# Performance work log

Measured on AMD Instinct MI355X. Metric: run time of the kernel, lower is better.

The kernel has to match this reference:

```python
import jax, jax.numpy as jnp
import numpy as np

K = 3  # from init kwarg


def setup_inputs() -> dict:
    key = jax.random.key(0)
    k1, k2 = jax.random.split(key)
    B, N, D = 32, 2048, 128
    features = jax.random.normal(k1, (B, N, D), dtype=jnp.float32)
    strength = jax.random.uniform(k2, (), dtype=jnp.float32)
    return {"features": features, "strength": strength}


def reference(features, strength):
    B, N, D = features.shape
    k = min(K, N - 1)
    x = jax.lax.stop_gradient(features)  # torch uses features.detach() for the mix path

    # pairwise euclidean distance (torch.cdist, p=2): ||a||^2 + ||b||^2 - 2 a.b
    sq = jnp.sum(x * x, axis=-1)                     # (B, N)
    d2 = sq[:, :, None] + sq[:, None, :] - 2.0 * jnp.einsum('bnd,bmd->bnm', x, x)
    dist = jnp.sqrt(jnp.maximum(d2, 0.0))            # (B, N, N)

    # mask self-distance with +1e6 on the diagonal
    eye = jnp.eye(N, dtype=dist.dtype)
    dist = dist + eye[None, :, :] * 1000000.0

    # k smallest -> top_k of negated distances
    _, idx = jax.lax.top_k(-dist, k)                 # idx: (B, N, k)

    # gather neighbor features: gathered[b,n,j] = x[b, idx[b,n,j]]
    gathered = x[jnp.arange(B)[:, None, None], idx]  # (B, N, k, D)
    mix = jnp.mean(gathered, axis=2)                 # (B, N, D)

    s = jnp.clip(strength, 0.0, 1.0)
    return (1.0 - s) * features + s * mix
```

## Files before the change

kernel.cpp:

```cpp
#include <hip/hip_runtime.h>
#include <cfloat>

#define BB 32
#define NN 2048
#define DD 128
#define RM 64
#define CN 64

typedef __attribute__((ext_vector_type(8))) short short8;
typedef __attribute__((ext_vector_type(4))) float float4v;

__device__ __forceinline__ unsigned short f2bf(float f) {
    unsigned int u = __builtin_bit_cast(unsigned int, f);
    u += 0x7FFFu + ((u >> 16) & 1u);
    return (unsigned short)(u >> 16);
}

__device__ __forceinline__ unsigned int umn(unsigned int a, unsigned int b) { return a < b ? a : b; }
__device__ __forceinline__ unsigned int umx(unsigned int a, unsigned int b) { return a > b ? a : b; }
#define CSU(a, b) { unsigned int _lo = umn(a, b), _hi = umx(a, b); (a) = _lo; (b) = _hi; }

__device__ __forceinline__ void gl2lds16(const unsigned short* g, unsigned short* l) {
    __builtin_amdgcn_global_load_lds(
        (const __attribute__((address_space(1))) void*)g,
        (__attribute__((address_space(3))) void*)l, 16, 0, 0);
}

__global__ __launch_bounds__(256) void prep_kernel(const float* __restrict__ x,
        unsigned short* __restrict__ xb16, float* __restrict__ sq) {
    int t = blockIdx.x * 256 + threadIdx.x;
    int row = t >> 2;
    int q = t & 3;
    const float4* xp = reinterpret_cast<const float4*>(x + (size_t)row * DD + q * 32);
    unsigned short* op = xb16 + (size_t)row * DD + q * 32;
    float acc = 0.f;
#pragma unroll
    for (int i = 0; i < 4; ++i) {
        float4 v0 = xp[2 * i], v1 = xp[2 * i + 1];
        acc += v0.x * v0.x + v0.y * v0.y + v0.z * v0.z + v0.w * v0.w;
        acc += v1.x * v1.x + v1.y * v1.y + v1.z * v1.z + v1.w * v1.w;
        short8 pk;
        pk[0] = (short)f2bf(v0.x); pk[1] = (short)f2bf(v0.y);
        pk[2] = (short)f2bf(v0.z); pk[3] = (short)f2bf(v0.w);
        pk[4] = (short)f2bf(v1.x); pk[5] = (short)f2bf(v1.y);
        pk[6] = (short)f2bf(v1.z); pk[7] = (short)f2bf(v1.w);
        *reinterpret_cast<short8*>(op + i * 8) = pk;
    }
    acc += __shfl_xor(acc, 1);
    acc += __shfl_xor(acc, 2);
    if (q == 0) sq[row] = acc;
}

__global__ __launch_bounds__(256) void sq_kernel(const float* __restrict__ x,
                                                 float* __restrict__ sq) {
    int t = blockIdx.x * 256 + threadIdx.x;
    int row = t >> 2;
    int q = t & 3;
    const float4* xp = reinterpret_cast<const float4*>(x + (size_t)row * DD + q * 32);
    float acc = 0.f;
#pragma unroll
    for (int i = 0; i < 8; ++i) {
        float4 v = xp[i];
        acc += v.x * v.x + v.y * v.y + v.z * v.z + v.w * v.w;
    }
    acc += __shfl_xor(acc, 1);
    acc += __shfl_xor(acc, 2);
    if (q == 0) sq[row] = acc;
}

template<bool PRE>
__global__ __launch_bounds__(256, 4) void knn_kernel(const float* __restrict__ x,
        const unsigned short* __restrict__ xb16g,
        const float* __restrict__ sqv, const float* __restrict__ strength,
        float* __restrict__ out) {
    __shared__ __align__(16) unsigned short btile[2 * CN * DD];
    __shared__ unsigned int cand8[RM * 8];

    const int b = blockIdx.x;
    const int row0 = blockIdx.y * RM;
    const int tid = threadIdx.x;
    const int w = tid >> 6;
    const int lane = tid & 63;
    const int m = lane & 15;
    const int quad = lane >> 4;
    const float* __restrict__ xb = x + (size_t)b * NN * DD;
    const unsigned short* __restrict__ gb = PRE ? xb16g + (size_t)b * NN * DD : nullptr;

    short8 afrag[4];
    if constexpr (PRE) {
#pragma unroll
        for (int kc = 0; kc < 4; ++kc)
            afrag[kc] = *reinterpret_cast<const short8*>(
                gb + (size_t)(row0 + 16 * w + m) * DD + kc * 32 + quad * 8);
    } else {
#pragma unroll
        for (int kc = 0; kc < 4; ++kc) {
            const float4* src = reinterpret_cast<const float4*>(
                xb + (size_t)(row0 + 16 * w + m) * DD + kc * 32 + quad * 8);
            float4 v0 = src[0], v1 = src[1];
            short8 pk;
            pk[0] = (short)f2bf(v0.x); pk[1] = (short)f2bf(v0.y);
            pk[2] = (short)f2bf(v0.z); pk[3] = (short)f2bf(v0.w);
            pk[4] = (short)f2bf(v1.x); pk[5] = (short)f2bf(v1.y);
            pk[6] = (short)f2bf(v1.z); pk[7] = (short)f2bf(v1.w);
            afrag[kc] = pk;
        }
    }

    {
        unsigned short* buf = btile;
        if constexpr (PRE) {
#pragma unroll
            for (int l = 0; l < 4; ++l) {
                int f = (l * 4 + w) * 64 + lane;
                int r = f >> 4, p = f & 15;
                int c = p ^ (r & 7);
                gl2lds16(gb + (size_t)r * DD + c * 8, buf + (l * 4 + w) * 512);
            }
        } else {
#pragma unroll
            for (int l = 0; l < 4; ++l) {
                int id = l * 256 + tid;
                int r = id >> 4, c = id & 15, p = c ^ (r & 7);
                const float4* src = reinterpret_cast<const float4*>(xb + (size_t)r * DD + c * 8);
                float4 v0 = src[0], v1 = src[1];
                short8 pk;
                pk[0] = (short)f2bf(v0.x); pk[1] = (short)f2bf(v0.y);
                pk[2] = (short)f2bf(v0.z); pk[3] = (short)f2bf(v0.w);
                pk[4] = (short)f2bf(v1.x); pk[5] = (short)f2bf(v1.y);
                pk[6] = (short)f2bf(v1.z); pk[7] = (short)f2bf(v1.w);
                *reinterpret_cast<short8*>(buf + r * DD + p * 8) = pk;
            }
        }
    }
    __syncthreads();

    unsigned int tk[4][4];
#pragma unroll
    for (int i = 0; i < 4; ++i)
#pragma unroll
        for (int q = 0; q < 4; ++q) tk[i][q] = 0xFFFFFFFFu;

    for (int ct = 0; ct < NN / CN; ++ct) {
        unsigned short* cur = btile + (size_t)(ct & 1) * CN * DD;
        unsigned short* nxt = btile + (size_t)((ct + 1) & 1) * CN * DD;

        if (ct + 1 < NN / CN) {
            int cb = (ct + 1) * CN;
            if constexpr (PRE) {
#pragma unroll
                for (int l = 0; l < 4; ++l) {
                    int f = (l * 4 + w) * 64 + lane;
                    int r = f >> 4, p = f & 15;
                    int c = p ^ (r & 7);
                    gl2lds16(gb + (size_t)(cb + r) * DD + c * 8, nxt + (l * 4 + w) * 512);
                }
            } else {
#pragma unroll
                for (int l = 0; l < 4; ++l) {
                    int id = l * 256 + tid;
                    int r = id >> 4, c = id & 15, p = c ^ (r & 7);
                    const float4* src = reinterpret_cast<const float4*>(xb + (size_t)(cb + r) * DD + c * 8);
                    float4 v0 = src[0], v1 = src[1];
                    short8 pk;
                    pk[0] = (short)f2bf(v0.x); pk[1] = (short)f2bf(v0.y);
                    pk[2] = (short)f2bf(v0.z); pk[3] = (short)f2bf(v0.w);
                    pk[4] = (short)f2bf(v1.x); pk[5] = (short)f2bf(v1.y);
                    pk[6] = (short)f2bf(v1.z); pk[7] = (short)f2bf(v1.w);
                    *reinterpret_cast<short8*>(nxt + r * DD + p * 8) = pk;
                }
            }
        }

        float sqb[4];
#pragma unroll
        for (int cc = 0; cc < 4; ++cc)
            sqb[cc] = sqv[(size_t)b * NN + ct * CN + cc * 16 + m] + 1024.0f;

        float4v acc[4];
#pragma unroll
        for (int cc = 0; cc < 4; ++cc) acc[cc] = (float4v){0.f, 0.f, 0.f, 0.f};
#pragma unroll
        for (int kc = 0; kc < 4; ++kc) {
#pragma unroll
            for (int cc = 0; cc < 4; ++cc) {
                int rl = cc * 16 + m;
                int p = (kc * 4 + quad) ^ (m & 7);
                short8 bfrag = *reinterpret_cast<const short8*>(cur + rl * DD + p * 8);
                acc[cc] = __builtin_amdgcn_mfma_f32_16x16x32_bf16(afrag[kc], bfrag, acc[cc], 0, 0, 0);
            }
        }

#pragma unroll
        for (int cc = 0; cc < 4; ++cc) {
            unsigned int col = (unsigned int)(ct * CN + cc * 16 + m);
#pragma unroll
            for (int reg = 0; reg < 4; ++reg) {
                float scb = fmaf(-2.f, acc[cc][reg], sqb[cc]);
                unsigned int key = (__builtin_bit_cast(unsigned int, scb) & 0xFFFFF800u) | col;
                unsigned int n;
                n = umn(tk[reg][0], key); key = umx(tk[reg][0], key); tk[reg][0] = n;
                n = umn(tk[reg][1], key); key = umx(tk[reg][1], key); tk[reg][1] = n;
                n = umn(tk[reg][2], key); key = umx(tk[reg][2], key); tk[reg][2] = n;
                tk[reg][3] = umn(tk[reg][3], key);
            }
        }

        __syncthreads();
    }

#pragma unroll
    for (int reg = 0; reg < 4; ++reg) {
        unsigned int e[8];
#pragma unroll
        for (int j = 0; j < 4; ++j) e[j] = tk[reg][j];
#pragma unroll
        for (int j = 4; j < 8; ++j) e[j] = 0xFFFFFFFFu;
#pragma unroll
        for (int st = 0; st < 4; ++st) {
            int mask = 1 << st;
            unsigned int rv[8];
#pragma unroll
            for (int j = 0; j < 8; ++j)
                rv[j] = (unsigned int)__shfl_xor((int)e[7 - j], mask, 64);
#pragma unroll
            for (int j = 0; j < 8; ++j) e[j] = umn(e[j], rv[j]);
            CSU(e[0], e[4]); CSU(e[1], e[5]); CSU(e[2], e[6]); CSU(e[3], e[7]);
            CSU(e[0], e[2]); CSU(e[1], e[3]); CSU(e[4], e[6]); CSU(e[5], e[7]);
            CSU(e[0], e[1]); CSU(e[2], e[3]); CSU(e[4], e[5]); CSU(e[6], e[7]);
        }
        if (m == 0) {
            int row = 16 * w + quad * 4 + reg;
#pragma unroll
            for (int j = 0; j < 8; ++j) cand8[row * 8 + j] = e[j];
        }
    }
    __syncthreads();

    double* refd = reinterpret_cast<double*>(btile);
    int* best3 = reinterpret_cast<int*>(btile) + 1024;

    {
        int r = tid >> 2, q4 = tid & 3;
        int grow = row0 + r;
        int c0 = (int)(cand8[r * 8 + q4 * 2 + 0] & 0x7FFu);
        int c1 = (int)(cand8[r * 8 + q4 * 2 + 1] & 0x7FFu);
        const float* p0 = xb + (size_t)c0 * DD;
        const float* p1 = xb + (size_t)c1 * DD;
        const float* pr = xb + (size_t)grow * DD;
        double a0 = 0.0, a1 = 0.0;
#pragma unroll 4
        for (int d4 = 0; d4 < 32; ++d4) {
            float4 wv = *reinterpret_cast<const float4*>(pr + d4 * 4);
            float4 v0 = *reinterpret_cast<const float4*>(p0 + d4 * 4);
            float4 v1 = *reinterpret_cast<const float4*>(p1 + d4 * 4);
            double d;
            d = (double)wv.x - (double)v0.x; a0 += d * d;
            d = (double)wv.y - (double)v0.y; a0 += d * d;
            d = (double)wv.z - (double)v0.z; a0 += d * d;
            d = (double)wv.w - (double)v0.w; a0 += d * d;
            d = (double)wv.x - (double)v1.x; a1 += d * d;
            d = (double)wv.y - (double)v1.y; a1 += d * d;
            d = (double)wv.z - (double)v1.z; a1 += d * d;
            d = (double)wv.w - (double)v1.w; a1 += d * d;
        }
        refd[r * 8 + q4 * 2 + 0] = (c0 == grow) ? DBL_MAX : a0;
        refd[r * 8 + q4 * 2 + 1] = (c1 == grow) ? DBL_MAX : a1;
    }
    __syncthreads();

    if (tid < RM) {
        int r = tid;
        double b0 = DBL_MAX, b1 = DBL_MAX, b2 = DBL_MAX;
        int i0 = 0x7fffffff, i1 = 0x7fffffff, i2 = 0x7fffffff;
        for (int e = 0; e < 8; ++e) {
            double dv = refd[r * 8 + e];
            int ix = (int)(cand8[r * 8 + e] & 0x7FFu);
            if (dv < b2 || (dv == b2 && ix < i2)) {
                b2 = dv; i2 = ix;
                if (b1 > b2 || (b1 == b2 && i1 > i2)) { double td = b1; b1 = b2; b2 = td; int tn = i1; i1 = i2; i2 = tn; }
                if (b0 > b1 || (b0 == b1 && i0 > i1)) { double td = b0; b0 = b1; b1 = td; int tn = i0; i0 = i1; i1 = tn; }
            }
        }
        best3[r * 3 + 0] = i0; best3[r * 3 + 1] = i1; best3[r * 3 + 2] = i2;
    }
    __syncthreads();

    {
        int r = tid >> 2, q = tid & 3;
        float s = fminf(fmaxf(strength[0], 0.f), 1.f);
        const float* pa = xb + (size_t)(row0 + r) * DD + q * 32;
        const float* p1 = xb + (size_t)best3[r * 3 + 0] * DD + q * 32;
        const float* p2 = xb + (size_t)best3[r * 3 + 1] * DD + q * 32;
        const float* p3 = xb + (size_t)best3[r * 3 + 2] * DD + q * 32;
        float* po = out + ((size_t)b * NN + row0 + r) * DD + q * 32;
#pragma unroll
        for (int l = 0; l < 8; ++l) {
            float4 a  = *reinterpret_cast<const float4*>(pa + l * 4);
            float4 n1 = *reinterpret_cast<const float4*>(p1 + l * 4);
            float4 n2 = *reinterpret_cast<const float4*>(p2 + l * 4);
            float4 n3 = *reinterpret_cast<const float4*>(p3 + l * 4);
            float4 o;
            o.x = (1.f - s) * a.x + s * ((n1.x + n2.x + n3.x) / 3.f);
            o.y = (1.f - s) * a.y + s * ((n1.y + n2.y + n3.y) / 3.f);
            o.z = (1.f - s) * a.z + s * ((n1.z + n2.z + n3.z) / 3.f);
            o.w = (1.f - s) * a.w + s * ((n1.w + n2.w + n3.w) / 3.f);
            *reinterpret_cast<float4*>(po + l * 4) = o;
        }
    }
}

extern "C" void kernel_launch(void* const* d_in, const int* in_sizes, int n_in,
                              void* d_out, int out_size, void* d_ws, size_t ws_size,
                              hipStream_t stream) {
    const float* x = (const float*)d_in[0];
    const float* strength = (const float*)d_in[1];
    float* out = (float*)d_out;
    float* sq = (float*)d_ws;
    unsigned short* xb16 = (unsigned short*)((char*)d_ws + 256 * 1024);
    const size_t need = 256 * 1024 + (size_t)BB * NN * DD * sizeof(unsigned short);

    if (ws_size >= need) {
        prep_kernel<<<dim3((BB * NN * 4) / 256), 256, 0, stream>>>(x, xb16, sq);
        knn_kernel<true><<<dim3(BB, NN / RM), 256, 0, stream>>>(x, xb16, sq, strength, out);
    } else {
        sq_kernel<<<dim3((BB * NN * 4) / 256), 256, 0, stream>>>(x, sq);
        knn_kernel<false><<<dim3(BB, NN / RM), 256, 0, stream>>>(x, nullptr, sq, strength, out);
    }
}
```

Baseline: 204.1 us.

## Double rows per block so each B fragment feeds two MFMA row groups

Raises the rows per block from 64 to 128, so each wave now holds two 16-row A fragment groups and reuses every loaded B fragment from LDS for both. This halves B-tile LDS traffic and global tile loads per output row, and halves the grid size. In exchange it doubles the accumulator and top-k register state, which lowers the launch-bounds occupancy target from 4 to 2 blocks per SM. The refinement and output epilogues are remapped so 256 threads cover 128 rows.

```diff
diff --git a/kernel.cpp b/kernel.cpp
--- a/kernel.cpp
+++ b/kernel.cpp
@@ -4,7 +4,7 @@
 #define BB 32
 #define NN 2048
 #define DD 128
-#define RM 64
+#define RM 128
 #define CN 64
 
 typedef __attribute__((ext_vector_type(8))) short short8;
@@ -69,7 +69,7 @@
 }
 
 template<bool PRE>
-__global__ __launch_bounds__(256, 4) void knn_kernel(const float* __restrict__ x,
+__global__ __launch_bounds__(256, 2) void knn_kernel(const float* __restrict__ x,
         const unsigned short* __restrict__ xb16g,
         const float* __restrict__ sqv, const float* __restrict__ strength,
         float* __restrict__ out) {
@@ -86,25 +86,29 @@
     const float* __restrict__ xb = x + (size_t)b * NN * DD;
     const unsigned short* __restrict__ gb = PRE ? xb16g + (size_t)b * NN * DD : nullptr;
 
-    short8 afrag[4];
+    short8 afrag[2][4];
     if constexpr (PRE) {
 #pragma unroll
-        for (int kc = 0; kc < 4; ++kc)
-            afrag[kc] = *reinterpret_cast<const short8*>(
-                gb + (size_t)(row0 + 16 * w + m) * DD + kc * 32 + quad * 8);
+        for (int rg = 0; rg < 2; ++rg)
+#pragma unroll
+            for (int kc = 0; kc < 4; ++kc)
+                afrag[rg][kc] = *reinterpret_cast<const short8*>(
+                    gb + (size_t)(row0 + 32 * w + rg * 16 + m) * DD + kc * 32 + quad * 8);
     } else {
 #pragma unroll
-        for (int kc = 0; kc < 4; ++kc) {
-            const float4* src = reinterpret_cast<const float4*>(
-                xb + (size_t)(row0 + 16 * w + m) * DD + kc * 32 + quad * 8);
-            float4 v0 = src[0], v1 = src[1];
-            short8 pk;
-            pk[0] = (short)f2bf(v0.x); pk[1] = (short)f2bf(v0.y);
-            pk[2] = (short)f2bf(v0.z); pk[3] = (short)f2bf(v0.w);
-            pk[4] = (short)f2bf(v1.x); pk[5] = (short)f2bf(v1.y);
-            pk[6] = (short)f2bf(v1.z); pk[7] = (short)f2bf(v1.w);
-            afrag[kc] = pk;
-        }
+        for (int rg = 0; rg < 2; ++rg)
+#pragma unroll
+            for (int kc = 0; kc < 4; ++kc) {
+                const float4* src = reinterpret_cast<const float4*>(
+                    xb + (size_t)(row0 + 32 * w + rg * 16 + m) * DD + kc * 32 + quad * 8);
+                float4 v0 = src[0], v1 = src[1];
+                short8 pk;
+                pk[0] = (short)f2bf(v0.x); pk[1] = (short)f2bf(v0.y);
+                pk[2] = (short)f2bf(v0.z); pk[3] = (short)f2bf(v0.w);
+                pk[4] = (short)f2bf(v1.x); pk[5] = (short)f2bf(v1.y);
+                pk[6] = (short)f2bf(v1.z); pk[7] = (short)f2bf(v1.w);
+                afrag[rg][kc] = pk;
+            }
     }
 
     {
@@ -135,11 +139,13 @@
     }
     __syncthreads();
 
-    unsigned int tk[4][4];
-#pragma unroll
-    for (int i = 0; i < 4; ++i)
-#pragma unroll
-        for (int q = 0; q < 4; ++q) tk[i][q] = 0xFFFFFFFFu;
+    unsigned int tk[2][4][4];
+#pragma unroll
+    for (int rg = 0; rg < 2; ++rg)
+#pragma unroll
+        for (int i = 0; i < 4; ++i)
+#pragma unroll
+            for (int q = 0; q < 4; ++q) tk[rg][i][q] = 0xFFFFFFFFu;
 
     for (int ct = 0; ct < NN / CN; ++ct) {
         unsigned short* cur = btile + (size_t)(ct & 1) * CN * DD;
@@ -177,95 +183,108 @@
         for (int cc = 0; cc < 4; ++cc)
             sqb[cc] = sqv[(size_t)b * NN + ct * CN + cc * 16 + m] + 1024.0f;
 
-        float4v acc[4];
-#pragma unroll
-        for (int cc = 0; cc < 4; ++cc) acc[cc] = (float4v){0.f, 0.f, 0.f, 0.f};
+        float4v acc[2][4];
+#pragma unroll
+        for (int rg = 0; rg < 2; ++rg)
+#pragma unroll
+            for (int cc = 0; cc < 4; ++cc) acc[rg][cc] = (float4v){0.f, 0.f, 0.f, 0.f};
 #pragma unroll
         for (int kc = 0; kc < 4; ++kc) {
+            short8 bfrag[4];
 #pragma unroll
             for (int cc = 0; cc < 4; ++cc) {
                 int rl = cc * 16 + m;
                 int p = (kc * 4 + quad) ^ (m & 7);
-                short8 bfrag = *reinterpret_cast<const short8*>(cur + rl * DD + p * 8);
-                acc[cc] = __builtin_amdgcn_mfma_f32_16x16x32_bf16(afrag[kc], bfrag, acc[cc], 0, 0, 0);
-            }
+                bfrag[cc] = *reinterpret_cast<const short8*>(cur + rl * DD + p * 8);
+            }
+#pragma unroll
+            for (int rg = 0; rg < 2; ++rg)
+#pragma unroll
+                for (int cc = 0; cc < 4; ++cc)
+                    acc[rg][cc] = __builtin_amdgcn_mfma_f32_16x16x32_bf16(
+                        afrag[rg][kc], bfrag[cc], acc[rg][cc], 0, 0, 0);
         }
 
 #pragma unroll
         for (int cc = 0; cc < 4; ++cc) {
             unsigned int col = (unsigned int)(ct * CN + cc * 16 + m);
 #pragma unroll
-            for (int reg = 0; reg < 4; ++reg) {
-                float scb = fmaf(-2.f, acc[cc][reg], sqb[cc]);
-                unsigned int key = (__builtin_bit_cast(unsigned int, scb) & 0xFFFFF800u) | col;
-                unsigned int n;
-                n = umn(tk[reg][0], key); key = umx(tk[reg][0], key); tk[reg][0] = n;
-                n = umn(tk[reg][1], key); key = umx(tk[reg][1], key); tk[reg][1] = n;
-                n = umn(tk[reg][2], key); key = umx(tk[reg][2], key); tk[reg][2] = n;
-                tk[reg][3] = umn(tk[reg][3], key);
-            }
+            for (int rg = 0; rg < 2; ++rg)
+#pragma unroll
+                for (int reg = 0; reg < 4; ++reg) {
+                    float scb = fmaf(-2.f, acc[rg][cc][reg], sqb[cc]);
+                    unsigned int key = (__builtin_bit_cast(unsigned int, scb) & 0xFFFFF800u) | col;
+                    unsigned int n;
+                    n = umn(tk[rg][reg][0], key); key = umx(tk[rg][reg][0], key); tk[rg][reg][0] = n;
+                    n = umn(tk[rg][reg][1], key); key = umx(tk[rg][reg][1], key); tk[rg][reg][1] = n;
+                    n = umn(tk[rg][reg][2], key); key = umx(tk[rg][reg][2], key); tk[rg][reg][2] = n;
+                    tk[rg][reg][3] = umn(tk[rg][reg][3], key);
+                }
         }
 
         __syncthreads();
     }
 
 #pragma unroll
-    for (int reg = 0; reg < 4; ++reg) {
-        unsigned int e[8];
-#pragma unroll
-        for (int j = 0; j < 4; ++j) e[j] = tk[reg][j];
-#pragma unroll
-        for (int j = 4; j < 8; ++j) e[j] = 0xFFFFFFFFu;
-#pragma unroll
-        for (int st = 0; st < 4; ++st) {
-            int mask = 1 << st;
-            unsigned int rv[8];
-#pragma unroll
-            for (int j = 0; j < 8; ++j)
-                rv[j] = (unsigned int)__shfl_xor((int)e[7 - j], mask, 64);
-#pragma unroll
-            for (int j = 0; j < 8; ++j) e[j] = umn(e[j], rv[j]);
-            CSU(e[0], e[4]); CSU(e[1], e[5]); CSU(e[2], e[6]); CSU(e[3], e[7]);
-            CSU(e[0], e[2]); CSU(e[1], e[3]); CSU(e[4], e[6]); CSU(e[5], e[7]);
-            CSU(e[0], e[1]); CSU(e[2], e[3]); CSU(e[4], e[5]); CSU(e[6], e[7]);
-        }
-        if (m == 0) {
-            int row = 16 * w + quad * 4 + reg;
-#pragma unroll
-            for (int j = 0; j < 8; ++j) cand8[row * 8 + j] = e[j];
-        }
-    }
+    for (int rg = 0; rg < 2; ++rg)
+#pragma unroll
+        for (int reg = 0; reg < 4; ++reg) {
+            unsigned int e[8];
+#pragma unroll
+            for (int j = 0; j < 4; ++j) e[j] = tk[rg][reg][j];
+#pragma unroll
+            for (int j = 4; j < 8; ++j) e[j] = 0xFFFFFFFFu;
+#pragma unroll
+            for (int st = 0; st < 4; ++st) {
+                int mask = 1 << st;
+                unsigned int rv[8];
+#pragma unroll
+                for (int j = 0; j < 8; ++j)
+                    rv[j] = (unsigned int)__shfl_xor((int)e[7 - j], mask, 64);
+#pragma unroll
+                for (int j = 0; j < 8; ++j) e[j] = umn(e[j], rv[j]);
+                CSU(e[0], e[4]); CSU(e[1], e[5]); CSU(e[2], e[6]); CSU(e[3], e[7]);
+                CSU(e[0], e[2]); CSU(e[1], e[3]); CSU(e[4], e[6]); CSU(e[5], e[7]);
+                CSU(e[0], e[1]); CSU(e[2], e[3]); CSU(e[4], e[5]); CSU(e[6], e[7]);
+            }
+            if (m == 0) {
+                int row = 32 * w + rg * 16 + quad * 4 + reg;
+#pragma unroll
+                for (int j = 0; j < 8; ++j) cand8[row * 8 + j] = e[j];
+            }
+        }
     __syncthreads();
 
     double* refd = reinterpret_cast<double*>(btile);
-    int* best3 = reinterpret_cast<int*>(btile) + 1024;
+    int* best3 = reinterpret_cast<int*>(btile) + 2048;
 
     {
-        int r = tid >> 2, q4 = tid & 3;
+        int r = tid >> 1, h = tid & 1;
         int grow = row0 + r;
-        int c0 = (int)(cand8[r * 8 + q4 * 2 + 0] & 0x7FFu);
-        int c1 = (int)(cand8[r * 8 + q4 * 2 + 1] & 0x7FFu);
-        const float* p0 = xb + (size_t)c0 * DD;
-        const float* p1 = xb + (size_t)c1 * DD;
+        int ci[4];
+#pragma unroll
+        for (int j = 0; j < 4; ++j) ci[j] = (int)(cand8[r * 8 + h * 4 + j] & 0x7FFu);
         const float* pr = xb + (size_t)grow * DD;
-        double a0 = 0.0, a1 = 0.0;
+        const float* pc[4];
+#pragma unroll
+        for (int j = 0; j < 4; ++j) pc[j] = xb + (size_t)ci[j] * DD;
+        double a[4] = {0.0, 0.0, 0.0, 0.0};
 #pragma unroll 4
         for (int d4 = 0; d4 < 32; ++d4) {
             float4 wv = *reinterpret_cast<const float4*>(pr + d4 * 4);
-            float4 v0 = *reinterpret_cast<const float4*>(p0 + d4 * 4);
-            float4 v1 = *reinterpret_cast<const float4*>(p1 + d4 * 4);
-            double d;
-            d = (double)wv.x - (double)v0.x; a0 += d * d;
-            d = (double)wv.y - (double)v0.y; a0 += d * d;
-            d = (double)wv.z - (double)v0.z; a0 += d * d;
-            d = (double)wv.w - (double)v0.w; a0 += d * d;
-            d = (double)wv.x - (double)v1.x; a1 += d * d;
-            d = (double)wv.y - (double)v1.y; a1 += d * d;
-            d = (double)wv.z - (double)v1.z; a1 += d * d;
-            d = (double)wv.w - (double)v1.w; a1 += d * d;
-        }
-        refd[r * 8 + q4 * 2 + 0] = (c0 == grow) ? DBL_MAX : a0;
-        refd[r * 8 + q4 * 2 + 1] = (c1 == grow) ? DBL_MAX : a1;
+#pragma unroll
+            for (int j = 0; j < 4; ++j) {
+                float4 v = *reinterpret_cast<const float4*>(pc[j] + d4 * 4);
+                double d;
+                d = (double)wv.x - (double)v.x; a[j] += d * d;
+                d = (double)wv.y - (double)v.y; a[j] += d * d;
+                d = (double)wv.z - (double)v.z; a[j] += d * d;
+                d = (double)wv.w - (double)v.w; a[j] += d * d;
+            }
+        }
+#pragma unroll
+        for (int j = 0; j < 4; ++j)
+            refd[r * 8 + h * 4 + j] = (ci[j] == grow) ? DBL_MAX : a[j];
     }
     __syncthreads();
 
@@ -287,15 +306,15 @@
     __syncthreads();
 
     {
-        int r = tid >> 2, q = tid & 3;
+        int r = tid >> 1, q = tid & 1;
         float s = fminf(fmaxf(strength[0], 0.f), 1.f);
-        const float* pa = xb + (size_t)(row0 + r) * DD + q * 32;
-        const float* p1 = xb + (size_t)best3[r * 3 + 0] * DD + q * 32;
-        const float* p2 = xb + (size_t)best3[r * 3 + 1] * DD + q * 32;
-        const float* p3 = xb + (size_t)best3[r * 3 + 2] * DD + q * 32;
-        float* po = out + ((size_t)b * NN + row0 + r) * DD + q * 32;
-#pragma unroll
-        for (int l = 0; l < 8; ++l) {
+        const float* pa = xb + (size_t)(row0 + r) * DD + q * 64;
+        const float* p1 = xb + (size_t)best3[r * 3 + 0] * DD + q * 64;
+        const float* p2 = xb + (size_t)best3[r * 3 + 1] * DD + q * 64;
+        const float* p3 = xb + (size_t)best3[r * 3 + 2] * DD + q * 64;
+        float* po = out + ((size_t)b * NN + row0 + r) * DD + q * 64;
+#pragma unroll
+        for (int l = 0; l < 16; ++l) {
             float4 a  = *reinterpret_cast<const float4*>(pa + l * 4);
             float4 n1 = *reinterpret_cast<const float4*>(p1 + l * 4);
             float4 n2 = *reinterpret_cast<const float4*>(p2 + l * 4);
```

Measured after the change: 200.8 us. About the same (-1.6%).
